# Performance work log

Measured on AMD Instinct MI355X. Metric: run time of the kernel, lower is better.

Reference implementation:

```python
import jax, jax.numpy as jnp
import numpy as np

N, M, D = 8192, 8192, 512

def setup_inputs() -> dict:
    key = jax.random.key(0)
    kx, ky = jax.random.split(key)
    X = jax.random.normal(kx, (N, D), dtype=jnp.float32)
    Y = jax.random.normal(ky, (M, D), dtype=jnp.float32)
    gamma = jnp.float32(1.0)  # learnable scalar kernel width
    return {"X": X, "Y": Y, "gamma": gamma}

def reference(X, Y, gamma):
    # RBF kernel: exp(-gamma * ||x_i - y_j||^2)
    x2 = jnp.sum(X * X, axis=-1)            # [n]
    y2 = jnp.sum(Y * Y, axis=-1)            # [m]
    xy = jnp.einsum('nd,md->nm', X, Y)      # [n, m] GEMM
    sq = x2[:, None] + y2[None, :] - 2.0 * xy
    sq = jnp.maximum(sq, 0.0)               # clamp tiny negatives from fp error
    return jnp.exp(-gamma * sq)
```

## Files before the change

kernel.cpp:

```cpp
#include <hip/hip_runtime.h>
#include <hip/hip_bf16.h>


#define NROWS 8192
#define D_DIM 512
#define BM 256
#define BN 256
#define BK 64
#define NKT (D_DIM / BK)

using bf16x8 = __attribute__((ext_vector_type(8))) short;
using f32x4  = __attribute__((ext_vector_type(4))) float;

__device__ inline unsigned pack2_bf16(float a, float b) {
    unsigned ua = __builtin_bit_cast(unsigned, a);
    unsigned ub = __builtin_bit_cast(unsigned, b);
    ua = (ua + 0x7fffu + ((ua >> 16) & 1u)) >> 16;
    ub = (ub + 0x7fffu + ((ub >> 16) & 1u)) >> 16;
    return ua | (ub << 16);
}

__global__ __launch_bounds__(64) void prep_all(const float* __restrict__ X,
                                               const float* __restrict__ Y,
                                               unsigned short* __restrict__ Xb,
                                               unsigned short* __restrict__ Yb,
                                               float* __restrict__ x2,
                                               float* __restrict__ y2) {
    const int bid  = blockIdx.x;
    const bool isY = bid >= NROWS;
    const int row  = isY ? bid - NROWS : bid;
    const float* src = isY ? Y : X;
    unsigned short* dst = isY ? Yb : Xb;
    float* nrm = isY ? y2 : x2;

    const int lane = threadIdx.x;
    const float4* s = reinterpret_cast<const float4*>(src) + (size_t)row * (D_DIM / 4);
    float4 v0 = s[lane * 2];
    float4 v1 = s[lane * 2 + 1];
    float ss = v0.x * v0.x + v0.y * v0.y + v0.z * v0.z + v0.w * v0.w +
               v1.x * v1.x + v1.y * v1.y + v1.z * v1.z + v1.w * v1.w;
    uint4 p;
    p.x = pack2_bf16(v0.x, v0.y);
    p.y = pack2_bf16(v0.z, v0.w);
    p.z = pack2_bf16(v1.x, v1.y);
    p.w = pack2_bf16(v1.z, v1.w);
    reinterpret_cast<uint4*>(dst + (size_t)row * D_DIM)[lane] = p;
    #pragma unroll
    for (int off = 32; off; off >>= 1) ss += __shfl_down(ss, off);
    if (lane == 0) nrm[row] = ss;
}

__device__ inline void gload_lds16(const unsigned short* g, unsigned short* l) {
    __builtin_amdgcn_global_load_lds(
        (const __attribute__((address_space(1))) void*)g,
        (__attribute__((address_space(3))) void*)l, 16, 0, 0);
}

#define VMCNT(n) asm volatile("s_waitcnt vmcnt(" #n ")" ::: "memory")
#define BAR()    asm volatile("s_barrier" ::: "memory")
#define LDF(p)   (*reinterpret_cast<const bf16x8*>(p))
#define MFMA(a, b, c) __builtin_amdgcn_mfma_f32_16x16x32_bf16(a, b, c, 0, 0, 0)

__global__ __launch_bounds__(512, 2) void rbf_gemm(
    const unsigned short* __restrict__ Xb, const unsigned short* __restrict__ Yb,
    const float* __restrict__ x2, const float* __restrict__ y2,
    const float* __restrict__ gptr, float* __restrict__ out) {
    __shared__ unsigned short sA[2][BM * BK];
    __shared__ unsigned short sB[2][BN * BK];

    const int bid  = blockIdx.x;
    const int xcd  = bid & 7;
    const int idx  = bid >> 3;
    const int rnd  = idx >> 5;
    const int pos  = idx & 31;
    const int st   = rnd * 8 + xcd;
    const int brow = (st & 3) * 8 + (pos >> 2);
    const int bcol = (st >> 2) * 4 + (pos & 3);

    const int tid  = threadIdx.x;
    const int lane = tid & 63;
    const int wid  = tid >> 6;
    const int wr   = wid >> 2;
    const int wc   = wid & 3;

    const int slot  = tid & 7;
    const int srowA = tid >> 3;
    const int srowB = ((tid >> 3) & 31) + ((tid >> 8) << 6);
    const int scol  = (slot ^ ((tid >> 3) & 7)) * 8;
    const unsigned short* gA = Xb + (size_t)(brow * BM + srowA) * D_DIM + scol;
    const unsigned short* gB = Yb + (size_t)(bcol * BN + srowB) * D_DIM + scol;
    const int loffA = srowA * BK + slot * 8;
    const int loffB = srowB * BK + slot * 8;

    auto stA = [&](int d, int kt, int odd) {
        const unsigned short* g = gA + (size_t)(odd * 64) * D_DIM + kt * BK;
        unsigned short* l = sA[d] + odd * 64 * BK + loffA;
        gload_lds16(g, l);
        gload_lds16(g + 128 * D_DIM, l + 128 * BK);
    };
    auto stB = [&](int d, int kt, int odd) {
        const unsigned short* g = gB + (size_t)(odd * 32) * D_DIM + kt * BK;
        unsigned short* l = sB[d] + odd * 32 * BK + loffB;
        gload_lds16(g, l);
        gload_lds16(g + 128 * D_DIM, l + 128 * BK);
    };
    auto STAGE_S = [&](int s) {
        if (s >= 4 * NKT) return;
        const int kt = s >> 2, ht = s & 3, d = kt & 1;
        if      (ht == 0) stA(d, kt, 0);
        else if (ht == 1) stB(d, kt, 0);
        else if (ht == 2) stB(d, kt, 1);
        else              stA(d, kt, 1);
    };

    const int lr  = lane & 15;
    const int kg  = lane >> 4;
    const int lx  = lane & 7;
    const int sl0 = ((0 * 4 + kg) ^ lx) * 8;
    const int sl1 = ((1 * 4 + kg) ^ lx) * 8;
    const int aBase = (wr * 128 + lr) * BK;
    const int bBase = (wc * 64 + lr) * BK;

    f32x4 acc[8][4] = {};
    bf16x8 av[4][2], bv[4][2];

    #pragma unroll
    for (int s = 0; s < 7; ++s) STAGE_S(s);
    VMCNT(6);
    BAR();

    for (int t = 0; t < NKT; ++t) {
        const int c = t & 1;
        const unsigned short* A = sA[c];
        const unsigned short* B = sB[c];
        const int sbase = 7 + 4 * t;

        #pragma unroll
        for (int m = 0; m < 4; ++m) {
            av[m][0] = LDF(A + aBase + m * 16 * BK + sl0);
            av[m][1] = LDF(A + aBase + m * 16 * BK + sl1);
        }
        #pragma unroll
        for (int n = 0; n < 2; ++n) {
            bv[n][0] = LDF(B + bBase + n * 16 * BK + sl0);
            bv[n][1] = LDF(B + bBase + n * 16 * BK + sl1);
        }
        STAGE_S(sbase);
        BAR();
        __builtin_amdgcn_s_setprio(1);
        #pragma unroll
        for (int m = 0; m < 4; ++m)
            #pragma unroll
            for (int n = 0; n < 2; ++n) {
                acc[m][n] = MFMA(av[m][0], bv[n][0], acc[m][n]);
                acc[m][n] = MFMA(av[m][1], bv[n][1], acc[m][n]);
            }
        __builtin_amdgcn_s_setprio(0);
        BAR();

        #pragma unroll
        for (int n = 2; n < 4; ++n) {
            bv[n][0] = LDF(B + bBase + n * 16 * BK + sl0);
            bv[n][1] = LDF(B + bBase + n * 16 * BK + sl1);
        }
        STAGE_S(sbase + 1);
        BAR();
        __builtin_amdgcn_s_setprio(1);
        #pragma unroll
        for (int m = 0; m < 4; ++m)
            #pragma unroll
            for (int n = 2; n < 4; ++n) {
                acc[m][n] = MFMA(av[m][0], bv[n][0], acc[m][n]);
                acc[m][n] = MFMA(av[m][1], bv[n][1], acc[m][n]);
            }
        __builtin_amdgcn_s_setprio(0);
        BAR();

        #pragma unroll
        for (int m = 0; m < 4; ++m) {
            av[m][0] = LDF(A + aBase + (m + 4) * 16 * BK + sl0);
            av[m][1] = LDF(A + aBase + (m + 4) * 16 * BK + sl1);
        }
        STAGE_S(sbase + 2);
        BAR();
        __builtin_amdgcn_s_setprio(1);
        #pragma unroll
        for (int m = 0; m < 4; ++m)
            #pragma unroll
            for (int n = 0; n < 2; ++n) {
                acc[m + 4][n] = MFMA(av[m][0], bv[n][0], acc[m + 4][n]);
                acc[m + 4][n] = MFMA(av[m][1], bv[n][1], acc[m + 4][n]);
            }
        __builtin_amdgcn_s_setprio(0);
        BAR();

        STAGE_S(sbase + 3);
        if (t < NKT - 2)       VMCNT(6);
        else if (t == NKT - 2) VMCNT(0);
        BAR();
        __builtin_amdgcn_s_setprio(1);
        #pragma unroll
        for (int m = 0; m < 4; ++m)
            #pragma unroll
            for (int n = 2; n < 4; ++n) {
                acc[m + 4][n] = MFMA(av[m][0], bv[n][0], acc[m + 4][n]);
                acc[m + 4][n] = MFMA(av[m][1], bv[n][1], acc[m + 4][n]);
            }
        __builtin_amdgcn_s_setprio(0);
        BAR();
    }

    const float g = *gptr;
    const int rbase = brow * BM + wr * 128 + (kg << 2);
    const int cbase = bcol * BN + wc * 64 + lr;

    float yv[4];
    #pragma unroll
    for (int n = 0; n < 4; ++n) yv[n] = y2[cbase + n * 16];

    #pragma unroll
    for (int m = 0; m < 8; ++m) {
        #pragma unroll
        for (int r = 0; r < 4; ++r) {
            const float xr = x2[rbase + m * 16 + r];
            const size_t ro = (size_t)(rbase + m * 16 + r) * NROWS + cbase;
            #pragma unroll
            for (int n = 0; n < 4; ++n) {
                float sq = fmaxf(xr + yv[n] - 2.0f * acc[m][n][r], 0.0f);
                __builtin_nontemporal_store(__expf(-g * sq), &out[ro + n * 16]);
            }
        }
    }
}

extern "C" void kernel_launch(void* const* d_in, const int* in_sizes, int n_in,
                              void* d_out, int out_size, void* d_ws, size_t ws_size,
                              hipStream_t stream) {
    const float* X = (const float*)d_in[0];
    const float* Y = (const float*)d_in[1];
    const float* gamma = (const float*)d_in[2];
    float* out = (float*)d_out;

    unsigned short* Xb = (unsigned short*)d_ws;
    unsigned short* Yb = Xb + (size_t)NROWS * D_DIM;
    float* x2 = (float*)(Yb + (size_t)NROWS * D_DIM);
    float* y2 = x2 + NROWS;

    prep_all<<<2 * NROWS, 64, 0, stream>>>(X, Y, Xb, Yb, x2, y2);

    const int grid = (NROWS / BM) * (NROWS / BN);
    rbf_gemm<<<grid, 512, 0, stream>>>(Xb, Yb, x2, y2, gamma, out);
}
```

Baseline: 392.7 us.

## Switch RBF GEMM operands to FP8 e4m3 with triple-buffered LDS staging

The prep kernel now quantizes X and Y to FP8 e4m3 instead of bf16, and writes them in a swizzled column order. The GEMM uses fp8 MFMA instructions with 16-byte LDS fragment loads and a three-stage LDS ring buffer, which deepens prefetch and changes the vmcnt schedule. This halves operand bytes moved from global memory and LDS. In exchange it adds notable quantization error to the dot products, which is only tolerable because the outputs mostly underflow to zero.

Result: no change. 393.6 us (+0.2%).

```diff
diff --git a/kernel.cpp b/kernel.cpp
--- a/kernel.cpp
+++ b/kernel.cpp
@@ -7,50 +7,72 @@
 #define BM 256
 #define BN 256
 #define BK 64
-#define NKT (D_DIM / BK)
-
-using bf16x8 = __attribute__((ext_vector_type(8))) short;
-using f32x4  = __attribute__((ext_vector_type(4))) float;
-
-__device__ inline unsigned pack2_bf16(float a, float b) {
-    unsigned ua = __builtin_bit_cast(unsigned, a);
-    unsigned ub = __builtin_bit_cast(unsigned, b);
-    ua = (ua + 0x7fffu + ((ua >> 16) & 1u)) >> 16;
-    ub = (ub + 0x7fffu + ((ub >> 16) & 1u)) >> 16;
-    return ua | (ub << 16);
+#define NKT 8
+#define TILEB (BM * BK)
+
+using f32x4 = __attribute__((ext_vector_type(4))) float;
+using i64x2 = __attribute__((ext_vector_type(2))) long;
+
+__device__ inline unsigned char f32_to_e4m3_1(float x) {
+    unsigned u = __builtin_bit_cast(unsigned, x);
+    unsigned s = (u >> 24) & 0x80u;
+    float ax = __builtin_fabsf(x);
+    if (ax < 0.015625f) {
+        int d = (int)rintf(ax * 512.0f);
+        return (unsigned char)(s | (d == 8 ? 0x08u : (unsigned)d));
+    }
+    if (ax >= 448.0f) return (unsigned char)(s | 0x7Eu);
+    unsigned r = u + 0x7FFFFu + ((u >> 20) & 1u);
+    unsigned e8 = ((r >> 23) & 0xFFu) - 120u;
+    unsigned m3 = (r >> 20) & 7u;
+    return (unsigned char)(s | (e8 << 3) | m3);
+}
+
+__device__ inline unsigned cvt_pk4_e4m3(float a, float b, float c, float d) {
+#if __has_builtin(__builtin_amdgcn_cvt_pk_fp8_f32)
+    int v = __builtin_amdgcn_cvt_pk_fp8_f32(a, b, 0, false);
+    v = __builtin_amdgcn_cvt_pk_fp8_f32(c, d, v, true);
+    return (unsigned)v;
+#else
+    return (unsigned)f32_to_e4m3_1(a) | ((unsigned)f32_to_e4m3_1(b) << 8) |
+           ((unsigned)f32_to_e4m3_1(c) << 16) | ((unsigned)f32_to_e4m3_1(d) << 24);
+#endif
 }
 
 __global__ __launch_bounds__(64) void prep_all(const float* __restrict__ X,
                                                const float* __restrict__ Y,
-                                               unsigned short* __restrict__ Xb,
-                                               unsigned short* __restrict__ Yb,
+                                               unsigned char* __restrict__ Xb,
+                                               unsigned char* __restrict__ Yb,
                                                float* __restrict__ x2,
                                                float* __restrict__ y2) {
     const int bid  = blockIdx.x;
     const bool isY = bid >= NROWS;
     const int row  = isY ? bid - NROWS : bid;
     const float* src = isY ? Y : X;
-    unsigned short* dst = isY ? Yb : Xb;
+    unsigned char* dst = isY ? Yb : Xb;
     float* nrm = isY ? y2 : x2;
 
-    const int lane = threadIdx.x;
-    const float4* s = reinterpret_cast<const float4*>(src) + (size_t)row * (D_DIM / 4);
-    float4 v0 = s[lane * 2];
-    float4 v1 = s[lane * 2 + 1];
-    float ss = v0.x * v0.x + v0.y * v0.y + v0.z * v0.z + v0.w * v0.w +
-               v1.x * v1.x + v1.y * v1.y + v1.z * v1.z + v1.w * v1.w;
-    uint4 p;
-    p.x = pack2_bf16(v0.x, v0.y);
-    p.y = pack2_bf16(v0.z, v0.w);
-    p.z = pack2_bf16(v1.x, v1.y);
-    p.w = pack2_bf16(v1.z, v1.w);
-    reinterpret_cast<uint4*>(dst + (size_t)row * D_DIM)[lane] = p;
+    const int l  = threadIdx.x;
+    const int c  = l >> 3;
+    const int p  = (l >> 1) & 3;
+    const int s  = l & 1;
+    const int xr = (row >> 1) & 3;
+    const int sc = c * 64 + s * 32 + ((p ^ xr) << 3);
+
+    const float4* sp = reinterpret_cast<const float4*>(src + (size_t)row * D_DIM + sc);
+    float4 a = sp[0], b = sp[1];
+    float ss = a.x*a.x + a.y*a.y + a.z*a.z + a.w*a.w +
+               b.x*b.x + b.y*b.y + b.z*b.z + b.w*b.w;
+    uint2 o;
+    o.x = cvt_pk4_e4m3(a.x, a.y, a.z, a.w);
+    o.y = cvt_pk4_e4m3(b.x, b.y, b.z, b.w);
+    reinterpret_cast<uint2*>(dst + (size_t)row * D_DIM)[l] = o;
     #pragma unroll
     for (int off = 32; off; off >>= 1) ss += __shfl_down(ss, off);
-    if (lane == 0) nrm[row] = ss;
-}
-
-__device__ inline void gload_lds16(const unsigned short* g, unsigned short* l) {
+    if (l == 0) nrm[row] = ss;
+}
+
+__device__ inline void gload_lds16(const unsigned char* g, unsigned char* l) {
     __builtin_amdgcn_global_load_lds(
         (const __attribute__((address_space(1))) void*)g,
         (__attribute__((address_space(3))) void*)l, 16, 0, 0);
@@ -58,15 +80,14 @@
 
 #define VMCNT(n) asm volatile("s_waitcnt vmcnt(" #n ")" ::: "memory")
 #define BAR()    asm volatile("s_barrier" ::: "memory")
-#define LDF(p)   (*reinterpret_cast<const bf16x8*>(p))
-#define MFMA(a, b, c) __builtin_amdgcn_mfma_f32_16x16x32_bf16(a, b, c, 0, 0, 0)
+#define MFMA8(a, b, c) __builtin_amdgcn_mfma_f32_16x16x32_fp8_fp8(a, b, c, 0, 0, 0)
 
 __global__ __launch_bounds__(512, 2) void rbf_gemm(
-    const unsigned short* __restrict__ Xb, const unsigned short* __restrict__ Yb,
+    const unsigned char* __restrict__ Xb, const unsigned char* __restrict__ Yb,
     const float* __restrict__ x2, const float* __restrict__ y2,
     const float* __restrict__ gptr, float* __restrict__ out) {
-    __shared__ unsigned short sA[2][BM * BK];
-    __shared__ unsigned short sB[2][BN * BK];
+    __shared__ __align__(16) unsigned char sA[3 * TILEB];
+    __shared__ __align__(16) unsigned char sB[3 * TILEB];
 
     const int bid  = blockIdx.x;
     const int xcd  = bid & 7;
@@ -83,128 +104,110 @@
     const int wr   = wid >> 2;
     const int wc   = wid & 3;
 
-    const int slot  = tid & 7;
-    const int srowA = tid >> 3;
-    const int srowB = ((tid >> 3) & 31) + ((tid >> 8) << 6);
-    const int scol  = (slot ^ ((tid >> 3) & 7)) * 8;
-    const unsigned short* gA = Xb + (size_t)(brow * BM + srowA) * D_DIM + scol;
-    const unsigned short* gB = Yb + (size_t)(bcol * BN + srowB) * D_DIM + scol;
-    const int loffA = srowA * BK + slot * 8;
-    const int loffB = srowB * BK + slot * 8;
-
-    auto stA = [&](int d, int kt, int odd) {
-        const unsigned short* g = gA + (size_t)(odd * 64) * D_DIM + kt * BK;
-        unsigned short* l = sA[d] + odd * 64 * BK + loffA;
-        gload_lds16(g, l);
-        gload_lds16(g + 128 * D_DIM, l + 128 * BK);
-    };
-    auto stB = [&](int d, int kt, int odd) {
-        const unsigned short* g = gB + (size_t)(odd * 32) * D_DIM + kt * BK;
-        unsigned short* l = sB[d] + odd * 32 * BK + loffB;
-        gload_lds16(g, l);
-        gload_lds16(g + 128 * D_DIM, l + 128 * BK);
-    };
+    const int slot  = tid & 3;
+    const int row64 = tid >> 2;
+    const int rgA0  = (row64 & 63) + ((row64 >> 6) << 7);
+    const int rgB0  = (row64 & 31) + (((row64 >> 5) & 1) << 6) + ((row64 >> 6) << 7);
+    const unsigned char* srcA0 = Xb + (size_t)(brow * BM + rgA0) * D_DIM + slot * 16;
+    const unsigned char* srcA1 = srcA0 + (size_t)64 * D_DIM;
+    const unsigned char* srcB0 = Yb + (size_t)(bcol * BN + rgB0) * D_DIM + slot * 16;
+    const unsigned char* srcB1 = srcB0 + (size_t)32 * D_DIM;
+    const int lA0 = rgA0 * BK + slot * 16, lA1 = lA0 + 64 * BK;
+    const int lB0 = rgB0 * BK + slot * 16, lB1 = lB0 + 32 * BK;
+
     auto STAGE_S = [&](int s) {
         if (s >= 4 * NKT) return;
-        const int kt = s >> 2, ht = s & 3, d = kt & 1;
-        if      (ht == 0) stA(d, kt, 0);
-        else if (ht == 1) stB(d, kt, 0);
-        else if (ht == 2) stB(d, kt, 1);
-        else              stA(d, kt, 1);
+        const int kt = s >> 2, ht = s & 3;
+        const int ab = (kt % 3) * TILEB;
+        const int ko = kt * BK;
+        if      (ht == 0) gload_lds16(srcA0 + ko, sA + ab + lA0);
+        else if (ht == 1) gload_lds16(srcB0 + ko, sB + ab + lB0);
+        else if (ht == 2) gload_lds16(srcB1 + ko, sB + ab + lB1);
+        else              gload_lds16(srcA1 + ko, sA + ab + lA1);
     };
 
-    const int lr  = lane & 15;
-    const int kg  = lane >> 4;
-    const int lx  = lane & 7;
-    const int sl0 = ((0 * 4 + kg) ^ lx) * 8;
-    const int sl1 = ((1 * 4 + kg) ^ lx) * 8;
-    const int aBase = (wr * 128 + lr) * BK;
-    const int bBase = (wc * 64 + lr) * BK;
+    const int lr   = lane & 15;
+    const int kg   = lane >> 4;
+    const int koff = (kg ^ ((lr >> 1) & 3)) << 4;
+    const int aOff = (wr * 128 + lr) * BK + koff;
+    const int bOff = (wc * 64  + lr) * BK + koff;
 
     f32x4 acc[8][4] = {};
-    bf16x8 av[4][2], bv[4][2];
-
-    #pragma unroll
-    for (int s = 0; s < 7; ++s) STAGE_S(s);
-    VMCNT(6);
+    i64x2 av[4], bv[4];
+
+    #pragma unroll
+    for (int s = 0; s < 9; ++s) STAGE_S(s);
+    VMCNT(5);
     BAR();
 
     for (int t = 0; t < NKT; ++t) {
-        const int c = t & 1;
-        const unsigned short* A = sA[c];
-        const unsigned short* B = sB[c];
-        const int sbase = 7 + 4 * t;
-
-        #pragma unroll
-        for (int m = 0; m < 4; ++m) {
-            av[m][0] = LDF(A + aBase + m * 16 * BK + sl0);
-            av[m][1] = LDF(A + aBase + m * 16 * BK + sl1);
-        }
-        #pragma unroll
-        for (int n = 0; n < 2; ++n) {
-            bv[n][0] = LDF(B + bBase + n * 16 * BK + sl0);
-            bv[n][1] = LDF(B + bBase + n * 16 * BK + sl1);
-        }
-        STAGE_S(sbase);
+        const unsigned char* A = sA + (t % 3) * TILEB;
+        const unsigned char* B = sB + (t % 3) * TILEB;
+        const int sb = 9 + 4 * t;
+
+        #pragma unroll
+        for (int m = 0; m < 4; ++m)
+            av[m] = *reinterpret_cast<const i64x2*>(A + aOff + m * 16 * BK);
+        #pragma unroll
+        for (int n = 0; n < 2; ++n)
+            bv[n] = *reinterpret_cast<const i64x2*>(B + bOff + n * 16 * BK);
+        STAGE_S(sb);
         BAR();
         __builtin_amdgcn_s_setprio(1);
         #pragma unroll
         for (int m = 0; m < 4; ++m)
             #pragma unroll
             for (int n = 0; n < 2; ++n) {
-                acc[m][n] = MFMA(av[m][0], bv[n][0], acc[m][n]);
-                acc[m][n] = MFMA(av[m][1], bv[n][1], acc[m][n]);
-            }
-        __builtin_amdgcn_s_setprio(0);
-        BAR();
-
-        #pragma unroll
-        for (int n = 2; n < 4; ++n) {
-            bv[n][0] = LDF(B + bBase + n * 16 * BK + sl0);
-            bv[n][1] = LDF(B + bBase + n * 16 * BK + sl1);
-        }
-        STAGE_S(sbase + 1);
+                acc[m][n] = MFMA8(av[m][0], bv[n][0], acc[m][n]);
+                acc[m][n] = MFMA8(av[m][1], bv[n][1], acc[m][n]);
+            }
+        __builtin_amdgcn_s_setprio(0);
+        BAR();
+
+        #pragma unroll
+        for (int n = 2; n < 4; ++n)
+            bv[n] = *reinterpret_cast<const i64x2*>(B + bOff + n * 16 * BK);
+        STAGE_S(sb + 1);
         BAR();
         __builtin_amdgcn_s_setprio(1);
         #pragma unroll
         for (int m = 0; m < 4; ++m)
             #pragma unroll
             for (int n = 2; n < 4; ++n) {
-                acc[m][n] = MFMA(av[m][0], bv[n][0], acc[m][n]);
-                acc[m][n] = MFMA(av[m][1], bv[n][1], acc[m][n]);
-            }
-        __builtin_amdgcn_s_setprio(0);
-        BAR();
-
-        #pragma unroll
-        for (int m = 0; m < 4; ++m) {
-            av[m][0] = LDF(A + aBase + (m + 4) * 16 * BK + sl0);
-            av[m][1] = LDF(A + aBase + (m + 4) * 16 * BK + sl1);
-        }
-        STAGE_S(sbase + 2);
+                acc[m][n] = MFMA8(av[m][0], bv[n][0], acc[m][n]);
+                acc[m][n] = MFMA8(av[m][1], bv[n][1], acc[m][n]);
+            }
+        __builtin_amdgcn_s_setprio(0);
+        BAR();
+
+        #pragma unroll
+        for (int m = 0; m < 4; ++m)
+            av[m] = *reinterpret_cast<const i64x2*>(A + aOff + (m + 4) * 16 * BK);
+        STAGE_S(sb + 2);
         BAR();
         __builtin_amdgcn_s_setprio(1);
         #pragma unroll
         for (int m = 0; m < 4; ++m)
             #pragma unroll
             for (int n = 0; n < 2; ++n) {
-                acc[m + 4][n] = MFMA(av[m][0], bv[n][0], acc[m + 4][n]);
-                acc[m + 4][n] = MFMA(av[m][1], bv[n][1], acc[m + 4][n]);
-            }
-        __builtin_amdgcn_s_setprio(0);
-        BAR();
-
-        STAGE_S(sbase + 3);
-        if (t < NKT - 2)       VMCNT(6);
-        else if (t == NKT - 2) VMCNT(0);
+                acc[m + 4][n] = MFMA8(av[m][0], bv[n][0], acc[m + 4][n]);
+                acc[m + 4][n] = MFMA8(av[m][1], bv[n][1], acc[m + 4][n]);
+            }
+        __builtin_amdgcn_s_setprio(0);
+        BAR();
+
+        STAGE_S(sb + 3);
+        if (t <= 4)      VMCNT(5);
+        else if (t == 5) VMCNT(4);
+        else if (t == 6) VMCNT(0);
         BAR();
         __builtin_amdgcn_s_setprio(1);
         #pragma unroll
         for (int m = 0; m < 4; ++m)
             #pragma unroll
             for (int n = 2; n < 4; ++n) {
-                acc[m + 4][n] = MFMA(av[m][0], bv[n][0], acc[m + 4][n]);
-                acc[m + 4][n] = MFMA(av[m][1], bv[n][1], acc[m + 4][n]);
+                acc[m + 4][n] = MFMA8(av[m][0], bv[n][0], acc[m + 4][n]);
+                acc[m + 4][n] = MFMA8(av[m][1], bv[n][1], acc[m + 4][n]);
             }
         __builtin_amdgcn_s_setprio(0);
         BAR();
@@ -241,8 +244,8 @@
     const float* gamma = (const float*)d_in[2];
     float* out = (float*)d_out;
 
-    unsigned short* Xb = (unsigned short*)d_ws;
-    unsigned short* Yb = Xb + (size_t)NROWS * D_DIM;
+    unsigned char* Xb = (unsigned char*)d_ws;
+    unsigned char* Yb = Xb + (size_t)NROWS * D_DIM;
     float* x2 = (float*)(Yb + (size_t)NROWS * D_DIM);
     float* y2 = x2 + NROWS;
 
```
